# Performance work log

Hardware: AMD Instinct MI355X
Metric: run time of the kernel (lower is better)

## Reference

```python
import jax, jax.numpy as jnp
import numpy as np

B, T, C = 4, 2048, 1024
E, I, K = 8, 1408, 2
N_SHARED = 1
IS = I * N_SHARED  # shared expert intermediate size


def setup_inputs() -> dict:
    key = jax.random.key(0)
    ks = jax.random.split(key, 8)
    s = 0.02
    return {
        "x": jax.random.normal(ks[0], (B, T, C), dtype=jnp.float32),
        "Wg": jax.random.normal(ks[1], (E, C), dtype=jnp.float32) * s,   # gate: Linear(C->E), weight [out,in]
        "W1": jax.random.normal(ks[2], (E, I, C), dtype=jnp.float32) * s,  # fc_1 per expert
        "W2": jax.random.normal(ks[3], (E, I, C), dtype=jnp.float32) * s,  # fc_2 per expert
        "W3": jax.random.normal(ks[4], (E, C, I), dtype=jnp.float32) * s,  # proj per expert
        "Ws1": jax.random.normal(ks[5], (IS, C), dtype=jnp.float32) * s,   # shared expert fc_1
        "Ws2": jax.random.normal(ks[6], (IS, C), dtype=jnp.float32) * s,   # shared expert fc_2
        "Ws3": jax.random.normal(ks[7], (C, IS), dtype=jnp.float32) * s,   # shared expert proj
    }


def reference(x, Wg, W1, W2, W3, Ws1, Ws2, Ws3):
    b, t, c = x.shape
    xf = x.reshape(-1, c)                       # [N, C]
    n = xf.shape[0]

    # Router: softmax in float32, top-k gating
    logits = xf @ Wg.T                          # [N, E]
    probs = jax.nn.softmax(logits.astype(jnp.float32), axis=-1)
    topk_p, topk_i = jax.lax.top_k(probs, K)    # [N, K]
    topk_p = topk_p.astype(x.dtype)

    # Dense combine weights: w[n, e] = sum_k topk_p[n, k] * (topk_i[n, k] == e)
    comb = jnp.zeros((n, E), dtype=x.dtype).at[jnp.arange(n)[:, None], topk_i].add(topk_p)

    # All experts on all tokens (dense equivalent of masked dispatch), weighted combine
    g = jnp.einsum('nc,eic->nei', xf, W1)       # [N, E, I]
    u = jnp.einsum('nc,eic->nei', xf, W2)       # [N, E, I]
    h = jax.nn.silu(g) * u                      # SwiGLU
    o = jnp.einsum('nei,eci->nec', h, W3)       # [N, E, C]
    y = jnp.einsum('nec,ne->nc', o, comb).reshape(b, t, c)

    # Shared expert on the residual input
    shared = (jax.nn.silu(x @ Ws1.T) * (x @ Ws2.T)) @ Ws3.T  # [B, T, C]
    return y + shared
```

## Files before the change

kernel.cpp:

```cpp
#include <hip/hip_runtime.h>
#include <stdint.h>

typedef __bf16 bf16;
typedef __attribute__((ext_vector_type(8))) __bf16 bf16x8;
typedef __attribute__((ext_vector_type(4))) float f32x4;

#define N_TOK 8192
#define C_DIM 1024
#define I_DIM 1408
#define NE 8
#define NEA 9
#define H_ROWS 25600

#define CNT_OFF   0
#define OFFS_OFF  64
#define TT_OFF    128
#define BTOK_OFF  192
#define BP_OFF    (BTOK_OFF + NE * N_TOK * 4)
#define ROUTER_END (BP_OFF + NE * N_TOK * 4)
#define TSEL_OFF  ROUTER_END
#define TP0_OFF   (TSEL_OFF + N_TOK * 4)
#define TP1_OFF   (TP0_OFF + N_TOK * 4)
#define XB_OFF    (1u << 20)
#define WB1_OFF   (18u << 20)
#define WB2_OFF   (43u << 20)
#define WB3_OFF   (68u << 20)
#define H_OFF     (93u << 20)

__device__ __forceinline__ void gload16(const void* g, void* l) {
  __builtin_amdgcn_global_load_lds(
      (const __attribute__((address_space(1))) void*)g,
      (__attribute__((address_space(3))) void*)l, 16, 0, 0);
}

#define SCHED() __builtin_amdgcn_sched_barrier(0)
#define BAR()   __builtin_amdgcn_s_barrier()
#define VM6()   asm volatile("s_waitcnt vmcnt(6)" ::: "memory")
#define VM0()   asm volatile("s_waitcnt vmcnt(0)" ::: "memory")

#define MM(AV, BV, H)                                                          \
  {                                                                            \
    __builtin_amdgcn_s_setprio(1);                                             \
    _Pragma("unroll") for (int q = 0; q < 4; ++q)                              \
        _Pragma("unroll") for (int nf = 0; nf < 4; ++nf)                       \
            acc[(H)*4 + q][nf] = __builtin_amdgcn_mfma_f32_16x16x32_bf16(      \
                AV[q], BV[nf], acc[(H)*4 + q][nf], 0, 0, 0);                   \
    __builtin_amdgcn_s_setprio(0);                                             \
  }

__global__ __launch_bounds__(256) void convert_kernel(
    const float* __restrict__ src, bf16* __restrict__ dst, int n8) {
  int i = blockIdx.x * 256 + threadIdx.x;
  if (i >= n8) return;
  const float* s = src + (size_t)i * 8;
  float4 a = *(const float4*)(s);
  float4 b = *(const float4*)(s + 4);
  bf16x8 v;
  v[0] = (bf16)a.x; v[1] = (bf16)a.y; v[2] = (bf16)a.z; v[3] = (bf16)a.w;
  v[4] = (bf16)b.x; v[5] = (bf16)b.y; v[6] = (bf16)b.z; v[7] = (bf16)b.w;
  *(bf16x8*)(dst + (size_t)i * 8) = v;
}

__global__ __launch_bounds__(256) void logits_kernel(
    const float* __restrict__ x, const float* __restrict__ Wg,
    int* __restrict__ tsel, float* __restrict__ tp0, float* __restrict__ tp1) {
  __shared__ __align__(16) float wg[NE * C_DIM];
  int t = threadIdx.x;
#pragma unroll
  for (int j = 0; j < 8; ++j) {
    int idx = (t + 256 * j) * 4;
    *(float4*)&wg[idx] = *(const float4*)&Wg[idx];
  }
  __syncthreads();
  int wid = t >> 6, lane = t & 63;
  int tok = blockIdx.x * 4 + wid;
  const float* xr = x + (size_t)tok * C_DIM;
  float acc[NE];
#pragma unroll
  for (int e = 0; e < NE; ++e) acc[e] = 0.f;
#pragma unroll
  for (int j = 0; j < 4; ++j) {
    int c4 = (lane + 64 * j) * 4;
    float4 xv = *(const float4*)&xr[c4];
#pragma unroll
    for (int e = 0; e < NE; ++e) {
      float4 wv = *(const float4*)&wg[e * C_DIM + c4];
      acc[e] += xv.x * wv.x + xv.y * wv.y + xv.z * wv.z + xv.w * wv.w;
    }
  }
  for (int o = 32; o >= 1; o >>= 1)
#pragma unroll
    for (int e = 0; e < NE; ++e) acc[e] += __shfl_xor(acc[e], o, 64);
  if (lane == 0) {
    float m = acc[0];
#pragma unroll
    for (int e = 1; e < NE; ++e) m = fmaxf(m, acc[e]);
    float p[NE], s = 0.f;
#pragma unroll
    for (int e = 0; e < NE; ++e) { p[e] = __expf(acc[e] - m); s += p[e]; }
    float inv = 1.f / s;
#pragma unroll
    for (int e = 0; e < NE; ++e) p[e] *= inv;
    int e0 = 0; float p0 = p[0];
#pragma unroll
    for (int e = 1; e < NE; ++e) if (p[e] > p0) { p0 = p[e]; e0 = e; }
    int e1 = -1; float p1 = -1.f;
#pragma unroll
    for (int e = 0; e < NE; ++e) {
      if (e == e0) continue;
      if (p[e] > p1) { p1 = p[e]; e1 = e; }
    }
    tsel[tok] = e0 | (e1 << 8);
    tp0[tok] = p0;
    tp1[tok] = p1;
  }
}

__global__ __launch_bounds__(1024) void bucketize_kernel(
    const int* __restrict__ tsel, const float* __restrict__ tp0,
    const float* __restrict__ tp1, int* __restrict__ cnt,
    int* __restrict__ btok, float* __restrict__ bp) {
  int e = blockIdx.x;
  int t = threadIdx.x;
  __shared__ int psum[1024];
  int sel[8], loc[8];
  int cntloc = 0;
  int base_tok = t * 8;
#pragma unroll
  for (int j = 0; j < 8; ++j) {
    int s = tsel[base_tok + j];
    int hit = ((s & 0xff) == e) ? 1 : ((((s >> 8) & 0xff) == e) ? 2 : 0);
    sel[j] = hit;
    loc[j] = cntloc;
    cntloc += (hit != 0);
  }
  psum[t] = cntloc;
  __syncthreads();
  for (int off = 1; off < 1024; off <<= 1) {
    int v = (t >= off) ? psum[t - off] : 0;
    __syncthreads();
    psum[t] += v;
    __syncthreads();
  }
  int excl = psum[t] - cntloc;
  if (t == 1023) cnt[e] = psum[1023];
#pragma unroll
  for (int j = 0; j < 8; ++j) {
    if (sel[j]) {
      int pos = excl + loc[j];
      int tok = base_tok + j;
      btok[e * N_TOK + pos] = tok;
      bp[e * N_TOK + pos] = (sel[j] == 1) ? tp0[tok] : tp1[tok];
    }
  }
}

__global__ void offsets_kernel(const int* __restrict__ cnt, int* __restrict__ offs,
                               int* __restrict__ tt) {
  if (threadIdx.x == 0) {
    int a = 0, b = 0;
    for (int e = 0; e < NE; ++e) {
      offs[e] = a; tt[e] = b;
      int pad = (cnt[e] + 127) & ~127;
      a += pad;
      b += (pad + 255) >> 8;
    }
    offs[NE] = a; tt[NE] = b;
  }
}

__device__ __forceinline__ int swz_off(int row, int kg) {
  return row * 64 + ((kg ^ ((row >> 1) & 3)) * 16);
}

__global__ __launch_bounds__(512) void stage1_kernel(
    const bf16* __restrict__ xb, const bf16* __restrict__ wb1,
    const bf16* __restrict__ wb2, const int* __restrict__ cnt,
    const int* __restrict__ offs, const int* __restrict__ tt,
    const int* __restrict__ btok, bf16* __restrict__ H) {
  int bid = blockIdx.x;
  int wgid = (bid & 7) * 154 + (bid >> 3);
  int tau = wgid % 112;
  int i0 = (wgid / 112) * 128;
  int e, row0, slotbase, limit;
  if (tau < 32) {
    e = NE; row0 = tau * 256; slotbase = 0; limit = N_TOK;
  } else {
    int tr = tau - 32;
    if (tr >= tt[NE]) return;
    e = NE - 1;
#pragma unroll
    for (int q = 0; q < NE; ++q) if (tr < tt[q + 1]) { e = q; break; }
    row0 = (tr - tt[e]) * 256;
    slotbase = N_TOK + offs[e];
    limit = cnt[e];
    if (row0 >= limit) return;
  }

  __shared__ __align__(16) char smem[131072];
  const int t = threadIdx.x;
  const int lane = t & 63, wid = t >> 6;
  const int wr = wid >> 2, wc = wid & 3;
  const int l15 = lane & 15, l4 = lane >> 4;

  const int srow = t >> 2;
  const int gsrc = (t & 3) ^ ((srow >> 1) & 3);
  int ar0 = row0 + srow, ar1 = row0 + srow + 128;
  int tok0, tok1;
  if (e == NE) { tok0 = ar0; tok1 = ar1; }
  else {
    int ix0 = e * N_TOK + (ar0 < N_TOK ? ar0 : N_TOK - 1);
    int ix1 = e * N_TOK + (ar1 < N_TOK ? ar1 : N_TOK - 1);
    tok0 = btok[ix0] & (N_TOK - 1);
    tok1 = btok[ix1] & (N_TOK - 1);
  }
  const bf16* asrc0 = xb + (size_t)tok0 * C_DIM + gsrc * 8;
  const bf16* asrc1 = xb + (size_t)tok1 * C_DIM + gsrc * 8;
  const bf16* bsrc0;
  const bf16* bsrc1;
  {
    int r = srow;
    int q = r >> 4, m = q >> 1, sel = q & 1;
    int irow = i0 + m * 16 + (r & 15);
    bsrc0 = (sel ? wb2 : wb1) + ((size_t)e * I_DIM + irow) * C_DIM + gsrc * 8;
    r = srow + 128;
    q = r >> 4; m = q >> 1; sel = q & 1;
    irow = i0 + m * 16 + (r & 15);
    bsrc1 = (sel ? wb2 : wb1) + ((size_t)e * I_DIM + irow) * C_DIM + gsrc * 8;
  }
  const int lo0 = t * 16;
  const int NKT = C_DIM / 32;

  auto stA = [&](int z) {
    if (z < NKT) {
      char* d = smem + (z & 3) * 32768;
      int k = z * 32;
      gload16(asrc0 + k, d + lo0);
      gload16(asrc1 + k, d + 8192 + lo0);
    }
  };
  auto stB = [&](int z) {
    if (z < NKT) {
      char* d = smem + (z & 3) * 32768 + 16384;
      int k = z * 32;
      gload16(bsrc0 + k, d + lo0);
      gload16(bsrc1 + k, d + 8192 + lo0);
    }
  };

  int aoff[8], boff[4];
#pragma unroll
  for (int mf = 0; mf < 8; ++mf) aoff[mf] = swz_off(wr * 128 + mf * 16 + l15, l4);
#pragma unroll
  for (int nf = 0; nf < 4; ++nf) boff[nf] = swz_off(wc * 64 + nf * 16 + l15, l4);

  f32x4 acc[8][4];
  f32x4 zero = {0.f, 0.f, 0.f, 0.f};
#pragma unroll
  for (int mf = 0; mf < 8; ++mf)
#pragma unroll
    for (int nf = 0; nf < 4; ++nf) acc[mf][nf] = zero;

  bf16x8 av0[4], av1[4], bv0[4], bv1[4];
  auto rdA = [&](bf16x8* dst, int T, int h) {
    char* base = smem + (T & 3) * 32768;
#pragma unroll
    for (int q = 0; q < 4; ++q) dst[q] = *(const bf16x8*)(base + aoff[h * 4 + q]);
  };
  auto rdB = [&](bf16x8* dst, int T) {
    char* base = smem + (T & 3) * 32768 + 16384;
#pragma unroll
    for (int nf = 0; nf < 4; ++nf) dst[nf] = *(const bf16x8*)(base + boff[nf]);
  };

  stB(0); stA(0); stB(1); stA(1); stB(2); stA(2);
  VM0();
  BAR();
  SCHED();
  rdA(av0, 0, 0); rdB(bv0, 0);

  const int NIT = NKT / 2;
  for (int it = 0; it < NIT; ++it) {
    int T0 = 2 * it, T1 = 2 * it + 1, T2n = 2 * it + 2;
    int zB = 2 * it + 3, zC = 2 * it + 4;
    rdA(av1, T0, 1);
    MM(av0, bv0, 0);
    stB(zB);
    SCHED(); VM6(); BAR(); SCHED();
    rdA(av0, T1, 0); rdB(bv1, T1);
    MM(av1, bv0, 1);
    stA(zB);
    SCHED(); BAR(); SCHED();
    rdA(av1, T1, 1);
    MM(av0, bv1, 0);
    stB(zC);
    SCHED(); VM6(); BAR(); SCHED();
    if (it + 1 < NIT) { rdA(av0, T2n, 0); rdB(bv0, T2n); }
    MM(av1, bv1, 1);
    stA(zC);
    SCHED(); BAR(); SCHED();
  }
  VM0();

#pragma unroll
  for (int mf = 0; mf < 8; ++mf)
#pragma unroll
    for (int r = 0; r < 4; ++r) {
      int rr = row0 + wr * 128 + mf * 16 + l4 * 4 + r;
      if (rr < limit) {
#pragma unroll
        for (int p = 0; p < 2; ++p) {
          float g = acc[mf][2 * p][r];
          float u = acc[mf][2 * p + 1][r];
          float h = (g / (1.f + __expf(-g))) * u;
          int col = i0 + (wc * 2 + p) * 16 + l15;
          H[(size_t)(slotbase + rr) * I_DIM + col] = (bf16)h;
        }
      }
    }
}

template <int SHARED>
__global__ __launch_bounds__(512) void stage2_kernel(
    const bf16* __restrict__ H, const bf16* __restrict__ wb3,
    const int* __restrict__ cnt, const int* __restrict__ offs,
    const int* __restrict__ tt, const int* __restrict__ btok,
    const float* __restrict__ bp, float* __restrict__ y) {
  int bid = blockIdx.x;
  int e, row0, slotbase, limit, c0;
  if (SHARED) {
    int wgid = (bid & 7) * 16 + (bid >> 3);
    e = NE; row0 = (wgid % 32) * 256; slotbase = 0; limit = N_TOK;
    c0 = (wgid / 32) * 256;
  } else {
    int wgid = (bid & 7) * 40 + (bid >> 3);
    int tr = wgid % 80;
    c0 = (wgid / 80) * 256;
    if (tr >= tt[NE]) return;
    e = NE - 1;
#pragma unroll
    for (int q = 0; q < NE; ++q) if (tr < tt[q + 1]) { e = q; break; }
    row0 = (tr - tt[e]) * 256;
    slotbase = N_TOK + offs[e];
    limit = cnt[e];
    if (row0 >= limit) return;
  }

  __shared__ __align__(16) char smem[131072];
  const int t = threadIdx.x;
  const int lane = t & 63, wid = t >> 6;
  const int wr = wid >> 2, wc = wid & 3;
  const int l15 = lane & 15, l4 = lane >> 4;

  const int srow = t >> 2;
  const int gsrc = (t & 3) ^ ((srow >> 1) & 3);
  int sr0 = slotbase + row0 + srow;        if (sr0 > H_ROWS - 1) sr0 = H_ROWS - 1;
  int sr1 = slotbase + row0 + srow + 128;  if (sr1 > H_ROWS - 1) sr1 = H_ROWS - 1;
  const bf16* asrc0 = H + (size_t)sr0 * I_DIM + gsrc * 8;
  const bf16* asrc1 = H + (size_t)sr1 * I_DIM + gsrc * 8;
  const bf16* bsrc0 = wb3 + ((size_t)e * C_DIM + c0 + srow) * I_DIM + gsrc * 8;
  const bf16* bsrc1 = bsrc0 + (size_t)128 * I_DIM;
  const int lo0 = t * 16;
  const int NKT = I_DIM / 32;

  auto stA = [&](int z) {
    if (z < NKT) {
      char* d = smem + (z & 3) * 32768;
      int k = z * 32;
      gload16(asrc0 + k, d + lo0);
      gload16(asrc1 + k, d + 8192 + lo0);
    }
  };
  auto stB = [&](int z) {
    if (z < NKT) {
      char* d = smem + (z & 3) * 32768 + 16384;
      int k = z * 32;
      gload16(bsrc0 + k, d + lo0);
      gload16(bsrc1 + k, d + 8192 + lo0);
    }
  };

  int aoff[8], boff[4];
#pragma unroll
  for (int mf = 0; mf < 8; ++mf) aoff[mf] = swz_off(wr * 128 + mf * 16 + l15, l4);
#pragma unroll
  for (int nf = 0; nf < 4; ++nf) boff[nf] = swz_off(wc * 64 + nf * 16 + l15, l4);

  f32x4 acc[8][4];
  f32x4 zero = {0.f, 0.f, 0.f, 0.f};
#pragma unroll
  for (int mf = 0; mf < 8; ++mf)
#pragma unroll
    for (int nf = 0; nf < 4; ++nf) acc[mf][nf] = zero;

  bf16x8 av0[4], av1[4], bv0[4], bv1[4];
  auto rdA = [&](bf16x8* dst, int T, int h) {
    char* base = smem + (T & 3) * 32768;
#pragma unroll
    for (int q = 0; q < 4; ++q) dst[q] = *(const bf16x8*)(base + aoff[h * 4 + q]);
  };
  auto rdB = [&](bf16x8* dst, int T) {
    char* base = smem + (T & 3) * 32768 + 16384;
#pragma unroll
    for (int nf = 0; nf < 4; ++nf) dst[nf] = *(const bf16x8*)(base + boff[nf]);
  };

  stB(0); stA(0); stB(1); stA(1); stB(2); stA(2);
  VM0();
  BAR();
  SCHED();
  rdA(av0, 0, 0); rdB(bv0, 0);

  const int NIT = NKT / 2;
  for (int it = 0; it < NIT; ++it) {
    int T0 = 2 * it, T1 = 2 * it + 1, T2n = 2 * it + 2;
    int zB = 2 * it + 3, zC = 2 * it + 4;
    rdA(av1, T0, 1);
    MM(av0, bv0, 0);
    stB(zB);
    SCHED(); VM6(); BAR(); SCHED();
    rdA(av0, T1, 0); rdB(bv1, T1);
    MM(av1, bv0, 1);
    stA(zB);
    SCHED(); BAR(); SCHED();
    rdA(av1, T1, 1);
    MM(av0, bv1, 0);
    stB(zC);
    SCHED(); VM6(); BAR(); SCHED();
    if (it + 1 < NIT) { rdA(av0, T2n, 0); rdB(bv0, T2n); }
    MM(av1, bv1, 1);
    stA(zC);
    SCHED(); BAR(); SCHED();
  }
  VM0();

#pragma unroll
  for (int mf = 0; mf < 8; ++mf)
#pragma unroll
    for (int r = 0; r < 4; ++r) {
      int idx = row0 + wr * 128 + mf * 16 + l4 * 4 + r;
      if (idx < limit) {
        if (SHARED) {
#pragma unroll
          for (int nf = 0; nf < 4; ++nf) {
            int col = c0 + wc * 64 + nf * 16 + l15;
            y[(size_t)idx * C_DIM + col] = acc[mf][nf][r];
          }
        } else {
          float p = bp[e * N_TOK + idx];
          int tok = btok[e * N_TOK + idx] & (N_TOK - 1);
#pragma unroll
          for (int nf = 0; nf < 4; ++nf) {
            int col = c0 + wc * 64 + nf * 16 + l15;
            atomicAdd(&y[(size_t)tok * C_DIM + col], p * acc[mf][nf][r]);
          }
        }
      }
    }
}

extern "C" void kernel_launch(void* const* d_in, const int* in_sizes, int n_in,
                              void* d_out, int out_size, void* d_ws, size_t ws_size,
                              hipStream_t stream) {
  const float* x = (const float*)d_in[0];
  const float* Wg = (const float*)d_in[1];
  const float* W1 = (const float*)d_in[2];
  const float* W2 = (const float*)d_in[3];
  const float* W3 = (const float*)d_in[4];
  const float* Ws1 = (const float*)d_in[5];
  const float* Ws2 = (const float*)d_in[6];
  const float* Ws3 = (const float*)d_in[7];
  float* y = (float*)d_out;
  char* ws = (char*)d_ws;

  int* cnt = (int*)(ws + CNT_OFF);
  int* offs = (int*)(ws + OFFS_OFF);
  int* tt = (int*)(ws + TT_OFF);
  int* btok = (int*)(ws + BTOK_OFF);
  float* bp = (float*)(ws + BP_OFF);
  int* tsel = (int*)(ws + TSEL_OFF);
  float* tp0 = (float*)(ws + TP0_OFF);
  float* tp1 = (float*)(ws + TP1_OFF);
  bf16* xb = (bf16*)(ws + XB_OFF);
  bf16* wb1 = (bf16*)(ws + WB1_OFF);
  bf16* wb2 = (bf16*)(ws + WB2_OFF);
  bf16* wb3 = (bf16*)(ws + WB3_OFF);
  bf16* H = (bf16*)(ws + H_OFF);

  hipMemsetAsync(ws, 0, ROUTER_END, stream);

  auto conv = [&](const float* s, bf16* d, size_t n) {
    int n8 = (int)(n / 8);
    convert_kernel<<<(n8 + 255) / 256, 256, 0, stream>>>(s, d, n8);
  };
  conv(x, xb, (size_t)N_TOK * C_DIM);
  conv(W1, wb1, (size_t)NE * I_DIM * C_DIM);
  conv(Ws1, wb1 + (size_t)NE * I_DIM * C_DIM, (size_t)I_DIM * C_DIM);
  conv(W2, wb2, (size_t)NE * I_DIM * C_DIM);
  conv(Ws2, wb2 + (size_t)NE * I_DIM * C_DIM, (size_t)I_DIM * C_DIM);
  conv(W3, wb3, (size_t)NE * C_DIM * I_DIM);
  conv(Ws3, wb3 + (size_t)NE * C_DIM * I_DIM, (size_t)C_DIM * I_DIM);

  logits_kernel<<<N_TOK / 4, 256, 0, stream>>>(x, Wg, tsel, tp0, tp1);
  bucketize_kernel<<<NE, 1024, 0, stream>>>(tsel, tp0, tp1, cnt, btok, bp);
  offsets_kernel<<<1, 64, 0, stream>>>(cnt, offs, tt);

  stage1_kernel<<<1232, 512, 0, stream>>>(xb, wb1, wb2, cnt, offs, tt, btok, H);
  stage2_kernel<1><<<128, 512, 0, stream>>>(H, wb3, cnt, offs, tt, btok, bp, y);
  stage2_kernel<0><<<320, 512, 0, stream>>>(H, wb3, cnt, offs, tt, btok, bp, y);
}
```

Baseline: 407.4 us.

## Merge A/B stage loads and use one barrier per k-tile in MoE GEMMs

Combines the separate A- and B-tile global-to-LDS loads into a single staging call per k-tile and reorganizes the software pipeline in both the gate/up and the down-projection GEMM kernels. Each k-tile now waits on vmcnt(4) and hits one barrier, where it used to hit two. LDS reads for the next tile are issued before that barrier, and the prologue no longer drains all loads. The aim is to cut synchronization stalls and keep MFMA issue denser. In exchange, the loads for a tile are issued in one burst and the timing of waits changes, which could expose more load latency.

```diff
diff --git a/kernel.cpp b/kernel.cpp
--- a/kernel.cpp
+++ b/kernel.cpp
@@ -35,7 +35,7 @@
 
 #define SCHED() __builtin_amdgcn_sched_barrier(0)
 #define BAR()   __builtin_amdgcn_s_barrier()
-#define VM6()   asm volatile("s_waitcnt vmcnt(6)" ::: "memory")
+#define VM4()   asm volatile("s_waitcnt vmcnt(4)" ::: "memory")
 #define VM0()   asm volatile("s_waitcnt vmcnt(0)" ::: "memory")
 
 #define MM(AV, BV, H)                                                          \
@@ -231,22 +231,16 @@
   const int lo0 = t * 16;
   const int NKT = C_DIM / 32;
 
-  auto stA = [&](int z) {
+  auto stAB = [&](int z) {
     if (z < NKT) {
       char* d = smem + (z & 3) * 32768;
       int k = z * 32;
+      gload16(bsrc0 + k, d + 16384 + lo0);
+      gload16(bsrc1 + k, d + 24576 + lo0);
       gload16(asrc0 + k, d + lo0);
       gload16(asrc1 + k, d + 8192 + lo0);
     }
   };
-  auto stB = [&](int z) {
-    if (z < NKT) {
-      char* d = smem + (z & 3) * 32768 + 16384;
-      int k = z * 32;
-      gload16(bsrc0 + k, d + lo0);
-      gload16(bsrc1 + k, d + 8192 + lo0);
-    }
-  };
 
   int aoff[8], boff[4];
 #pragma unroll
@@ -261,7 +255,7 @@
 #pragma unroll
     for (int nf = 0; nf < 4; ++nf) acc[mf][nf] = zero;
 
-  bf16x8 av0[4], av1[4], bv0[4], bv1[4];
+  bf16x8 av0[4], av1[4], bvA[4], bvB[4];
   auto rdA = [&](bf16x8* dst, int T, int h) {
     char* base = smem + (T & 3) * 32768;
 #pragma unroll
@@ -273,32 +267,25 @@
     for (int nf = 0; nf < 4; ++nf) dst[nf] = *(const bf16x8*)(base + boff[nf]);
   };
 
-  stB(0); stA(0); stB(1); stA(1); stB(2); stA(2);
-  VM0();
-  BAR();
-  SCHED();
-  rdA(av0, 0, 0); rdB(bv0, 0);
+  stAB(0); stAB(1); stAB(2);
+  SCHED(); VM4(); BAR(); SCHED();
+  rdA(av0, 0, 0); rdB(bvA, 0);
 
   const int NIT = NKT / 2;
   for (int it = 0; it < NIT; ++it) {
-    int T0 = 2 * it, T1 = 2 * it + 1, T2n = 2 * it + 2;
-    int zB = 2 * it + 3, zC = 2 * it + 4;
-    rdA(av1, T0, 1);
-    MM(av0, bv0, 0);
-    stB(zB);
-    SCHED(); VM6(); BAR(); SCHED();
-    rdA(av0, T1, 0); rdB(bv1, T1);
-    MM(av1, bv0, 1);
-    stA(zB);
-    SCHED(); BAR(); SCHED();
-    rdA(av1, T1, 1);
-    MM(av0, bv1, 0);
-    stB(zC);
-    SCHED(); VM6(); BAR(); SCHED();
-    if (it + 1 < NIT) { rdA(av0, T2n, 0); rdB(bv0, T2n); }
-    MM(av1, bv1, 1);
-    stA(zC);
-    SCHED(); BAR(); SCHED();
+    int z0 = 2 * it, z1 = 2 * it + 1;
+    stAB(z0 + 3);
+    rdA(av1, z0, 1);
+    MM(av0, bvA, 0);
+    rdA(av0, z1, 0); rdB(bvB, z1);
+    MM(av1, bvA, 1);
+    SCHED(); VM4(); BAR(); SCHED();
+    stAB(z1 + 3);
+    rdA(av1, z1, 1);
+    MM(av0, bvB, 0);
+    if (z1 + 1 < NKT) { rdA(av0, z1 + 1, 0); rdB(bvA, z1 + 1); }
+    MM(av1, bvB, 1);
+    SCHED(); VM4(); BAR(); SCHED();
   }
   VM0();
 
@@ -363,22 +350,16 @@
   const int lo0 = t * 16;
   const int NKT = I_DIM / 32;
 
-  auto stA = [&](int z) {
+  auto stAB = [&](int z) {
     if (z < NKT) {
       char* d = smem + (z & 3) * 32768;
       int k = z * 32;
+      gload16(bsrc0 + k, d + 16384 + lo0);
+      gload16(bsrc1 + k, d + 24576 + lo0);
       gload16(asrc0 + k, d + lo0);
       gload16(asrc1 + k, d + 8192 + lo0);
     }
   };
-  auto stB = [&](int z) {
-    if (z < NKT) {
-      char* d = smem + (z & 3) * 32768 + 16384;
-      int k = z * 32;
-      gload16(bsrc0 + k, d + lo0);
-      gload16(bsrc1 + k, d + 8192 + lo0);
-    }
-  };
 
   int aoff[8], boff[4];
 #pragma unroll
@@ -393,7 +374,7 @@
 #pragma unroll
     for (int nf = 0; nf < 4; ++nf) acc[mf][nf] = zero;
 
-  bf16x8 av0[4], av1[4], bv0[4], bv1[4];
+  bf16x8 av0[4], av1[4], bvA[4], bvB[4];
   auto rdA = [&](bf16x8* dst, int T, int h) {
     char* base = smem + (T & 3) * 32768;
 #pragma unroll
@@ -405,32 +386,25 @@
     for (int nf = 0; nf < 4; ++nf) dst[nf] = *(const bf16x8*)(base + boff[nf]);
   };
 
-  stB(0); stA(0); stB(1); stA(1); stB(2); stA(2);
-  VM0();
-  BAR();
-  SCHED();
-  rdA(av0, 0, 0); rdB(bv0, 0);
+  stAB(0); stAB(1); stAB(2);
+  SCHED(); VM4(); BAR(); SCHED();
+  rdA(av0, 0, 0); rdB(bvA, 0);
 
   const int NIT = NKT / 2;
   for (int it = 0; it < NIT; ++it) {
-    int T0 = 2 * it, T1 = 2 * it + 1, T2n = 2 * it + 2;
-    int zB = 2 * it + 3, zC = 2 * it + 4;
-    rdA(av1, T0, 1);
-    MM(av0, bv0, 0);
-    stB(zB);
-    SCHED(); VM6(); BAR(); SCHED();
-    rdA(av0, T1, 0); rdB(bv1, T1);
-    MM(av1, bv0, 1);
-    stA(zB);
-    SCHED(); BAR(); SCHED();
-    rdA(av1, T1, 1);
-    MM(av0, bv1, 0);
-    stB(zC);
-    SCHED(); VM6(); BAR(); SCHED();
-    if (it + 1 < NIT) { rdA(av0, T2n, 0); rdB(bv0, T2n); }
-    MM(av1, bv1, 1);
-    stA(zC);
-    SCHED(); BAR(); SCHED();
+    int z0 = 2 * it, z1 = 2 * it + 1;
+    stAB(z0 + 3);
+    rdA(av1, z0, 1);
+    MM(av0, bvA, 0);
+    rdA(av0, z1, 0); rdB(bvB, z1);
+    MM(av1, bvA, 1);
+    SCHED(); VM4(); BAR(); SCHED();
+    stAB(z1 + 3);
+    rdA(av1, z1, 1);
+    MM(av0, bvB, 0);
+    if (z1 + 1 < NKT) { rdA(av0, z1 + 1, 0); rdB(bvA, z1 + 1); }
+    MM(av1, bvB, 1);
+    SCHED(); VM4(); BAR(); SCHED();
   }
   VM0();
 
```

Measured after the change: 407.4 us. No clear change (+0.0%).

## Merge weight conversions into one kernel and fuse shared/routed stage2 launches

Applied to the files above, without the earlier changes.

Seven separate fp32-to-bf16 convert launches become one grid-stride kernel covering x and all weight tensors, which cuts launch overhead and tail gaps. The shared-expert and routed stage2 launches merge into one 448-block grid, so both kinds of tiles run concurrently instead of back to back. Because of the merge, the shared expert now writes through atomicAdd, so the whole output is zeroed with a memset first. The router workspace memset is dropped. The cost is the extra 32 MB memset of the output plus atomic traffic for the shared-expert writes.

```diff
diff --git a/kernel.cpp b/kernel.cpp
--- a/kernel.cpp
+++ b/kernel.cpp
@@ -48,17 +48,46 @@
     __builtin_amdgcn_s_setprio(0);                                             \
   }
 
-__global__ __launch_bounds__(256) void convert_kernel(
-    const float* __restrict__ src, bf16* __restrict__ dst, int n8) {
-  int i = blockIdx.x * 256 + threadIdx.x;
-  if (i >= n8) return;
-  const float* s = src + (size_t)i * 8;
-  float4 a = *(const float4*)(s);
-  float4 b = *(const float4*)(s + 4);
-  bf16x8 v;
-  v[0] = (bf16)a.x; v[1] = (bf16)a.y; v[2] = (bf16)a.z; v[3] = (bf16)a.w;
-  v[4] = (bf16)b.x; v[5] = (bf16)b.y; v[6] = (bf16)b.z; v[7] = (bf16)b.w;
-  *(bf16x8*)(dst + (size_t)i * 8) = v;
+#define C0 1048576
+#define C1 (C0 + 1441792)
+#define C2 (C1 + 180224)
+#define C3 (C2 + 1441792)
+#define C4 (C3 + 180224)
+#define C5 (C4 + 1441792)
+#define C6 (C5 + 180224)
+
+__global__ __launch_bounds__(256) void convert_all_kernel(
+    const float* __restrict__ x, const float* __restrict__ W1,
+    const float* __restrict__ Ws1, const float* __restrict__ W2,
+    const float* __restrict__ Ws2, const float* __restrict__ W3,
+    const float* __restrict__ Ws3, char* __restrict__ ws) {
+  for (int i = blockIdx.x * 256 + threadIdx.x; i < C6; i += gridDim.x * 256) {
+    const float* s;
+    bf16* d;
+    size_t off;
+    if (i < C0) {
+      s = x; d = (bf16*)(ws + XB_OFF); off = i;
+    } else if (i < C1) {
+      s = W1; d = (bf16*)(ws + WB1_OFF); off = i - C0;
+    } else if (i < C2) {
+      s = Ws1; d = (bf16*)(ws + WB1_OFF) + (size_t)NE * I_DIM * C_DIM; off = i - C1;
+    } else if (i < C3) {
+      s = W2; d = (bf16*)(ws + WB2_OFF); off = i - C2;
+    } else if (i < C4) {
+      s = Ws2; d = (bf16*)(ws + WB2_OFF) + (size_t)NE * I_DIM * C_DIM; off = i - C3;
+    } else if (i < C5) {
+      s = W3; d = (bf16*)(ws + WB3_OFF); off = i - C4;
+    } else {
+      s = Ws3; d = (bf16*)(ws + WB3_OFF) + (size_t)NE * C_DIM * I_DIM; off = i - C5;
+    }
+    const float* sp = s + off * 8;
+    float4 a = *(const float4*)(sp);
+    float4 b = *(const float4*)(sp + 4);
+    bf16x8 v;
+    v[0] = (bf16)a.x; v[1] = (bf16)a.y; v[2] = (bf16)a.z; v[3] = (bf16)a.w;
+    v[4] = (bf16)b.x; v[5] = (bf16)b.y; v[6] = (bf16)b.z; v[7] = (bf16)b.w;
+    *(bf16x8*)(d + off * 8) = v;
+  }
 }
 
 __global__ __launch_bounds__(256) void logits_kernel(
@@ -320,22 +349,21 @@
     }
 }
 
-template <int SHARED>
 __global__ __launch_bounds__(512) void stage2_kernel(
     const bf16* __restrict__ H, const bf16* __restrict__ wb3,
     const int* __restrict__ cnt, const int* __restrict__ offs,
     const int* __restrict__ tt, const int* __restrict__ btok,
     const float* __restrict__ bp, float* __restrict__ y) {
   int bid = blockIdx.x;
+  int wgid = (bid & 7) * 56 + (bid >> 3);
   int e, row0, slotbase, limit, c0;
-  if (SHARED) {
-    int wgid = (bid & 7) * 16 + (bid >> 3);
+  if (wgid < 128) {
     e = NE; row0 = (wgid % 32) * 256; slotbase = 0; limit = N_TOK;
     c0 = (wgid / 32) * 256;
   } else {
-    int wgid = (bid & 7) * 40 + (bid >> 3);
-    int tr = wgid % 80;
-    c0 = (wgid / 80) * 256;
+    int r = wgid - 128;
+    int tr = r % 80;
+    c0 = (r / 80) * 256;
     if (tr >= tt[NE]) return;
     e = NE - 1;
 #pragma unroll
@@ -440,20 +468,17 @@
     for (int r = 0; r < 4; ++r) {
       int idx = row0 + wr * 128 + mf * 16 + l4 * 4 + r;
       if (idx < limit) {
-        if (SHARED) {
-#pragma unroll
-          for (int nf = 0; nf < 4; ++nf) {
-            int col = c0 + wc * 64 + nf * 16 + l15;
-            y[(size_t)idx * C_DIM + col] = acc[mf][nf][r];
-          }
-        } else {
-          float p = bp[e * N_TOK + idx];
-          int tok = btok[e * N_TOK + idx] & (N_TOK - 1);
-#pragma unroll
-          for (int nf = 0; nf < 4; ++nf) {
-            int col = c0 + wc * 64 + nf * 16 + l15;
-            atomicAdd(&y[(size_t)tok * C_DIM + col], p * acc[mf][nf][r]);
-          }
+        float p;
+        int tok;
+        if (e == NE) { p = 1.f; tok = idx; }
+        else {
+          p = bp[e * N_TOK + idx];
+          tok = btok[e * N_TOK + idx] & (N_TOK - 1);
+        }
+#pragma unroll
+        for (int nf = 0; nf < 4; ++nf) {
+          int col = c0 + wc * 64 + nf * 16 + l15;
+          atomicAdd(&y[(size_t)tok * C_DIM + col], p * acc[mf][nf][r]);
         }
       }
     }
@@ -487,25 +512,14 @@
   bf16* wb3 = (bf16*)(ws + WB3_OFF);
   bf16* H = (bf16*)(ws + H_OFF);
 
-  hipMemsetAsync(ws, 0, ROUTER_END, stream);
-
-  auto conv = [&](const float* s, bf16* d, size_t n) {
-    int n8 = (int)(n / 8);
-    convert_kernel<<<(n8 + 255) / 256, 256, 0, stream>>>(s, d, n8);
-  };
-  conv(x, xb, (size_t)N_TOK * C_DIM);
-  conv(W1, wb1, (size_t)NE * I_DIM * C_DIM);
-  conv(Ws1, wb1 + (size_t)NE * I_DIM * C_DIM, (size_t)I_DIM * C_DIM);
-  conv(W2, wb2, (size_t)NE * I_DIM * C_DIM);
-  conv(Ws2, wb2 + (size_t)NE * I_DIM * C_DIM, (size_t)I_DIM * C_DIM);
-  conv(W3, wb3, (size_t)NE * C_DIM * I_DIM);
-  conv(Ws3, wb3 + (size_t)NE * C_DIM * I_DIM, (size_t)C_DIM * I_DIM);
+  hipMemsetAsync(y, 0, (size_t)N_TOK * C_DIM * 4, stream);
 
   logits_kernel<<<N_TOK / 4, 256, 0, stream>>>(x, Wg, tsel, tp0, tp1);
   bucketize_kernel<<<NE, 1024, 0, stream>>>(tsel, tp0, tp1, cnt, btok, bp);
   offsets_kernel<<<1, 64, 0, stream>>>(cnt, offs, tt);
 
+  convert_all_kernel<<<2048, 256, 0, stream>>>(x, W1, Ws1, W2, Ws2, W3, Ws3, ws);
+
   stage1_kernel<<<1232, 512, 0, stream>>>(xb, wb1, wb2, cnt, offs, tt, btok, H);
-  stage2_kernel<1><<<128, 512, 0, stream>>>(H, wb3, cnt, offs, tt, btok, bp, y);
-  stage2_kernel<0><<<320, 512, 0, stream>>>(H, wb3, cnt, offs, tt, btok, bp, y);
-}
+  stage2_kernel<<<448, 512, 0, stream>>>(H, wb3, cnt, offs, tt, btok, bp, y);
+}
```

Result: faster. 383.6 us (-5.8%).
